# Kernel tuning notes

Hardware: AMD Instinct MI355X
Metric: run time of the kernel (lower is better)

## Reference

```python
import jax, jax.numpy as jnp
import numpy as np

LN_EPS = 1e-5


def setup_inputs() -> dict:
    key = jax.random.key(0)
    ks = jax.random.split(key, 4)
    B, N, E, H = 2, 512, 128, 256
    h = jax.random.normal(ks[0], (B, N, E), dtype=jnp.float32)
    gamma = jnp.ones((E,), dtype=jnp.float32)
    beta = jnp.zeros((E,), dtype=jnp.float32)
    # First Linear: in_dim = 2E, out_dim = H. Stored as [2E, H] (x @ W1 + b1).
    W1 = jax.random.normal(ks[1], (2 * E, H), dtype=jnp.float32) / np.sqrt(2 * E)
    b1 = jnp.zeros((H,), dtype=jnp.float32)
    # Second Linear: [H, 1] squeezed to [H], scalar bias.
    w2 = jax.random.normal(ks[2], (H,), dtype=jnp.float32) / np.sqrt(H)
    b2 = jnp.zeros((), dtype=jnp.float32)
    return {"h": h, "gamma": gamma, "beta": beta, "W1": W1, "b1": b1,
            "w2": w2, "b2": b2}


def reference(h, gamma, beta, W1, b1, w2, b2):
    # LayerNorm over E
    mu = jnp.mean(h, axis=-1, keepdims=True)
    var = jnp.mean(jnp.square(h - mu), axis=-1, keepdims=True)
    h_n = (h - mu) * jax.lax.rsqrt(var + LN_EPS) * gamma + beta  # [B,N,E]

    E = h_n.shape[-1]
    # Decompose Linear(concat(h_i, h_j)) = h_i @ Wa + h_j @ Wb + b1
    Wa, Wb = W1[:E], W1[E:]
    a = jnp.einsum('bne,eh->bnh', h_n, Wa)  # contribution of first slot
    b = jnp.einsum('bne,eh->bnh', h_n, Wb)  # contribution of second slot
    # Pairwise pre-activation for the (i,j) ordering: [B,N,N,H]
    z_ij = a[:, :, None, :] + b[:, None, :, :] + b1
    g = jax.nn.gelu(z_ij, approximate=False)  # torch GELU is exact (erf)
    l_ij = jnp.einsum('bijh,h->bij', g, w2) + b2  # [B,N,N]
    # l_ji[b,i,j] == l_ij[b,j,i], so reuse via transpose (same math as
    # running the MLP twice on swapped concat order).
    return 0.5 * (l_ij + jnp.swapaxes(l_ij, 1, 2))
```

## Files before the change

### kernel.cpp

```cpp
#include <hip/hip_runtime.h>
#include <math.h>

#define EDIM 128
#define HDIM 256
#define NDIM 512
#define BDIM 2
#define LN_EPS 1e-5f

typedef float v2f __attribute__((ext_vector_type(2)));

__global__ __launch_bounds__(256) void k_ln_proj(
    const float* __restrict__ hptr, const float* __restrict__ gamma,
    const float* __restrict__ beta, const float* __restrict__ W1,
    const float* __restrict__ b1, float* __restrict__ a_out,
    float* __restrict__ b_out)
{
    __shared__ float hn_s[4][EDIM];
    const int tid = threadIdx.x;
    const int r = tid >> 6;
    const int lane = tid & 63;
    const int row0 = blockIdx.x * 4;
    const float2 v = *(const float2*)(hptr + (row0 + r) * EDIM + lane * 2);
    float s  = v.x + v.y;
    float ss = v.x * v.x + v.y * v.y;
    #pragma unroll
    for (int k = 32; k >= 1; k >>= 1) {
        s  += __shfl_xor(s, k, 64);
        ss += __shfl_xor(ss, k, 64);
    }
    const float mu  = s * (1.0f / EDIM);
    const float var = ss * (1.0f / EDIM) - mu * mu;
    const float rs  = rsqrtf(var + LN_EPS);
    const float2 g2 = *(const float2*)(gamma + lane * 2);
    const float2 be = *(const float2*)(beta + lane * 2);
    hn_s[r][lane * 2]     = (v.x - mu) * rs * g2.x + be.x;
    hn_s[r][lane * 2 + 1] = (v.y - mu) * rs * g2.y + be.y;
    __syncthreads();
    float sa0 = 0.f, sa1 = 0.f, sa2 = 0.f, sa3 = 0.f;
    float sb0 = 0.f, sb1 = 0.f, sb2 = 0.f, sb3 = 0.f;
    #pragma unroll 4
    for (int e = 0; e < EDIM; ++e) {
        const float wa = W1[e * HDIM + tid];
        const float wb = W1[(EDIM + e) * HDIM + tid];
        const float h0 = hn_s[0][e], h1 = hn_s[1][e];
        const float h2 = hn_s[2][e], h3 = hn_s[3][e];
        sa0 = fmaf(h0, wa, sa0); sa1 = fmaf(h1, wa, sa1);
        sa2 = fmaf(h2, wa, sa2); sa3 = fmaf(h3, wa, sa3);
        sb0 = fmaf(h0, wb, sb0); sb1 = fmaf(h1, wb, sb1);
        sb2 = fmaf(h2, wb, sb2); sb3 = fmaf(h3, wb, sb3);
    }
    const float bb1 = b1[tid];
    a_out[(row0 + 0) * HDIM + tid] = sa0;
    a_out[(row0 + 1) * HDIM + tid] = sa1;
    a_out[(row0 + 2) * HDIM + tid] = sa2;
    a_out[(row0 + 3) * HDIM + tid] = sa3;
    b_out[(row0 + 0) * HDIM + tid] = sb0 + bb1;
    b_out[(row0 + 1) * HDIM + tid] = sb1 + bb1;
    b_out[(row0 + 2) * HDIM + tid] = sb2 + bb1;
    b_out[(row0 + 3) * HDIM + tid] = sb3 + bb1;
}

__device__ __forceinline__ v2f gelu2(v2f z) {
    const v2f c2 = {-0.10294826f, -0.10294826f};
    const v2f c1 = {-2.3022082f, -2.3022082f};
    const v2f z2 = z * z;
    const v2f q  = __builtin_elementwise_fma(c2, z2, c1);
    const v2f p  = z * q;
    v2f e;
    e.x = __builtin_amdgcn_exp2f(p.x);
    e.y = __builtin_amdgcn_exp2f(p.y);
    const v2f d = e + 1.0f;
    v2f r;
    r.x = __builtin_amdgcn_rcpf(d.x);
    r.y = __builtin_amdgcn_rcpf(d.y);
    return z * r;
}

#define HHALF 128
#define PAD 132

__global__ __launch_bounds__(256) void k_pair(
    const float* __restrict__ a, const float* __restrict__ bpb,
    const float* __restrict__ w2, const float* __restrict__ b2,
    float* __restrict__ out)
{
    __shared__ float a_s[32][PAD];
    __shared__ float b_s[16][PAD];
    __shared__ float w2_s[HDIM];
    const int blk = blockIdx.x;
    const int bb = blk >> 9;
    const int bi = (blk >> 5) & 15;
    const int bj = blk & 31;
    const int tid = threadIdx.x;

    const float* arow = a + (bb * NDIM + bi * 32) * HDIM;
    const float* brow = bpb + (bb * NDIM + bj * 16) * HDIM;

    if (tid < HDIM / 4) ((float4*)w2_s)[tid] = ((const float4*)w2)[tid];

    const int ti = tid >> 4, tj = tid & 15;
    const float* ap0 = a_s[ti];
    const float* ap1 = a_s[ti + 16];
    const float* bp  = b_s[tj];
    v2f acc0 = {0.f, 0.f}, acc1 = {0.f, 0.f};

    #pragma unroll
    for (int half = 0; half < 2; ++half) {
        if (half) __syncthreads();
        #pragma unroll
        for (int idx = tid; idx < 1536; idx += 256) {
            if (idx < 1024) {
                const int r = idx >> 5, c = idx & 31;
                *(float4*)&a_s[r][c * 4] =
                    *(const float4*)(arow + r * HDIM + half * HHALF + c * 4);
            } else {
                const int k = idx - 1024;
                const int r = k >> 5, c = k & 31;
                *(float4*)&b_s[r][c * 4] =
                    *(const float4*)(brow + r * HDIM + half * HHALF + c * 4);
            }
        }
        __syncthreads();
        const float* wp = w2_s + half * HHALF;
        #pragma unroll 4
        for (int hh = 0; hh < HHALF; hh += 4) {
            const float4 a0 = *(const float4*)(ap0 + hh);
            const float4 a1 = *(const float4*)(ap1 + hh);
            const float4 b0 = *(const float4*)(bp + hh);
            const float4 wv = *(const float4*)(wp + hh);
            const v2f alo0 = {a0.x, a0.y}, ahi0 = {a0.z, a0.w};
            const v2f alo1 = {a1.x, a1.y}, ahi1 = {a1.z, a1.w};
            const v2f blo  = {b0.x, b0.y}, bhi  = {b0.z, b0.w};
            const v2f wlo  = {wv.x, wv.y}, whi  = {wv.z, wv.w};
            acc0 = __builtin_elementwise_fma(wlo, gelu2(alo0 + blo), acc0);
            acc0 = __builtin_elementwise_fma(whi, gelu2(ahi0 + bhi), acc0);
            acc1 = __builtin_elementwise_fma(wlo, gelu2(alo1 + blo), acc1);
            acc1 = __builtin_elementwise_fma(whi, gelu2(ahi1 + bhi), acc1);
        }
    }
    const float bias = b2[0];
    const int i0 = bi * 32 + ti;
    const int j0 = bj * 16 + tj;
    float* ob = out + (bb * NDIM + i0) * NDIM + j0;
    ob[0]         = acc0.x + acc0.y + bias;
    ob[16 * NDIM] = acc1.x + acc1.y + bias;
}

__global__ __launch_bounds__(256) void k_sym(float* __restrict__ out) {
    __shared__ float Ta[32][33];
    __shared__ float Tb[32][33];
    const int blk = blockIdx.x;
    const int b  = blk >> 8;
    const int ti = (blk >> 4) & 15;
    const int tj = blk & 15;
    if (tj < ti) return;
    float* base = out + b * NDIM * NDIM;
    const int tx = threadIdx.x & 31;
    const int ty = threadIdx.x >> 5;
    #pragma unroll
    for (int r = ty; r < 32; r += 8) {
        Ta[r][tx] = base[(ti * 32 + r) * NDIM + tj * 32 + tx];
        Tb[r][tx] = base[(tj * 32 + r) * NDIM + ti * 32 + tx];
    }
    __syncthreads();
    #pragma unroll
    for (int r = ty; r < 32; r += 8) {
        base[(ti * 32 + r) * NDIM + tj * 32 + tx] = 0.5f * (Ta[r][tx] + Tb[tx][r]);
    }
    if (ti != tj) {
        #pragma unroll
        for (int r = ty; r < 32; r += 8) {
            base[(tj * 32 + r) * NDIM + ti * 32 + tx] = 0.5f * (Tb[r][tx] + Ta[tx][r]);
        }
    }
}

extern "C" void kernel_launch(void* const* d_in, const int* in_sizes, int n_in,
                              void* d_out, int out_size, void* d_ws, size_t ws_size,
                              hipStream_t stream) {
    const float* hptr  = (const float*)d_in[0];
    const float* gamma = (const float*)d_in[1];
    const float* beta  = (const float*)d_in[2];
    const float* W1    = (const float*)d_in[3];
    const float* b1    = (const float*)d_in[4];
    const float* w2    = (const float*)d_in[5];
    const float* b2    = (const float*)d_in[6];
    float* out = (float*)d_out;

    float* a_ws = (float*)d_ws;
    float* b_ws = a_ws + BDIM * NDIM * HDIM;

    k_ln_proj<<<(BDIM * NDIM) / 4, 256, 0, stream>>>(hptr, gamma, beta, W1, b1, a_ws, b_ws);
    k_pair<<<BDIM * 512, 256, 0, stream>>>(a_ws, b_ws, w2, b2, out);
    k_sym<<<BDIM * 256, 256, 0, stream>>>(out);
}
```

Before: 49.23 us.

## Split pair kernel over hidden halves with atomic accumulation into zeroed output

Each pair block now handles only one half of the hidden dimension, doubling the grid to 2048 blocks. Partial sums are combined with atomicAdd into an output that is zeroed by a memset first, and the scalar bias moves into the symmetrisation kernel. The aim is more parallelism and occupancy, with one smem load and no mid-loop barrier per block. The cost is an extra memset, atomic traffic, and floating-point summation order that is no longer deterministic.

```diff
diff --git a/kernel.cpp b/kernel.cpp
--- a/kernel.cpp
+++ b/kernel.cpp
@@ -79,24 +79,38 @@
 #define HHALF 128
 #define PAD 132
 
-__global__ __launch_bounds__(256) void k_pair(
+__global__ __launch_bounds__(256, 6) void k_pair(
     const float* __restrict__ a, const float* __restrict__ bpb,
-    const float* __restrict__ w2, const float* __restrict__ b2,
-    float* __restrict__ out)
+    const float* __restrict__ w2, float* __restrict__ out)
 {
     __shared__ float a_s[32][PAD];
     __shared__ float b_s[16][PAD];
-    __shared__ float w2_s[HDIM];
+    __shared__ float w2_s[HHALF];
     const int blk = blockIdx.x;
-    const int bb = blk >> 9;
-    const int bi = (blk >> 5) & 15;
-    const int bj = blk & 31;
+    const int hh = blk & 1;
+    const int bj = (blk >> 1) & 31;
+    const int bi = (blk >> 6) & 15;
+    const int bb = blk >> 10;
     const int tid = threadIdx.x;
+    const int hho = hh * HHALF;
 
-    const float* arow = a + (bb * NDIM + bi * 32) * HDIM;
-    const float* brow = bpb + (bb * NDIM + bj * 16) * HDIM;
+    const float* arow = a + (bb * NDIM + bi * 32) * HDIM + hho;
+    const float* brow = bpb + (bb * NDIM + bj * 16) * HDIM + hho;
 
-    if (tid < HDIM / 4) ((float4*)w2_s)[tid] = ((const float4*)w2)[tid];
+    if (tid < HHALF / 4) ((float4*)w2_s)[tid] = ((const float4*)(w2 + hho))[tid];
+
+    #pragma unroll
+    for (int idx = tid; idx < 1536; idx += 256) {
+        if (idx < 1024) {
+            const int r = idx >> 5, c = idx & 31;
+            *(float4*)&a_s[r][c * 4] = *(const float4*)(arow + r * HDIM + c * 4);
+        } else {
+            const int k = idx - 1024;
+            const int r = k >> 5, c = k & 31;
+            *(float4*)&b_s[r][c * 4] = *(const float4*)(brow + r * HDIM + c * 4);
+        }
+    }
+    __syncthreads();
 
     const int ti = tid >> 4, tj = tid & 15;
     const float* ap0 = a_s[ti];
@@ -104,49 +118,30 @@
     const float* bp  = b_s[tj];
     v2f acc0 = {0.f, 0.f}, acc1 = {0.f, 0.f};
 
-    #pragma unroll
-    for (int half = 0; half < 2; ++half) {
-        if (half) __syncthreads();
-        #pragma unroll
-        for (int idx = tid; idx < 1536; idx += 256) {
-            if (idx < 1024) {
-                const int r = idx >> 5, c = idx & 31;
-                *(float4*)&a_s[r][c * 4] =
-                    *(const float4*)(arow + r * HDIM + half * HHALF + c * 4);
-            } else {
-                const int k = idx - 1024;
-                const int r = k >> 5, c = k & 31;
-                *(float4*)&b_s[r][c * 4] =
-                    *(const float4*)(brow + r * HDIM + half * HHALF + c * 4);
-            }
-        }
-        __syncthreads();
-        const float* wp = w2_s + half * HHALF;
-        #pragma unroll 4
-        for (int hh = 0; hh < HHALF; hh += 4) {
-            const float4 a0 = *(const float4*)(ap0 + hh);
-            const float4 a1 = *(const float4*)(ap1 + hh);
-            const float4 b0 = *(const float4*)(bp + hh);
-            const float4 wv = *(const float4*)(wp + hh);
-            const v2f alo0 = {a0.x, a0.y}, ahi0 = {a0.z, a0.w};
-            const v2f alo1 = {a1.x, a1.y}, ahi1 = {a1.z, a1.w};
-            const v2f blo  = {b0.x, b0.y}, bhi  = {b0.z, b0.w};
-            const v2f wlo  = {wv.x, wv.y}, whi  = {wv.z, wv.w};
-            acc0 = __builtin_elementwise_fma(wlo, gelu2(alo0 + blo), acc0);
-            acc0 = __builtin_elementwise_fma(whi, gelu2(ahi0 + bhi), acc0);
-            acc1 = __builtin_elementwise_fma(wlo, gelu2(alo1 + blo), acc1);
-            acc1 = __builtin_elementwise_fma(whi, gelu2(ahi1 + bhi), acc1);
-        }
+    #pragma unroll 4
+    for (int h4 = 0; h4 < HHALF; h4 += 4) {
+        const float4 a0 = *(const float4*)(ap0 + h4);
+        const float4 a1 = *(const float4*)(ap1 + h4);
+        const float4 b0 = *(const float4*)(bp + h4);
+        const float4 wv = *(const float4*)(w2_s + h4);
+        const v2f alo0 = {a0.x, a0.y}, ahi0 = {a0.z, a0.w};
+        const v2f alo1 = {a1.x, a1.y}, ahi1 = {a1.z, a1.w};
+        const v2f blo  = {b0.x, b0.y}, bhi  = {b0.z, b0.w};
+        const v2f wlo  = {wv.x, wv.y}, whi  = {wv.z, wv.w};
+        acc0 = __builtin_elementwise_fma(wlo, gelu2(alo0 + blo), acc0);
+        acc0 = __builtin_elementwise_fma(whi, gelu2(ahi0 + bhi), acc0);
+        acc1 = __builtin_elementwise_fma(wlo, gelu2(alo1 + blo), acc1);
+        acc1 = __builtin_elementwise_fma(whi, gelu2(ahi1 + bhi), acc1);
     }
-    const float bias = b2[0];
     const int i0 = bi * 32 + ti;
     const int j0 = bj * 16 + tj;
     float* ob = out + (bb * NDIM + i0) * NDIM + j0;
-    ob[0]         = acc0.x + acc0.y + bias;
-    ob[16 * NDIM] = acc1.x + acc1.y + bias;
+    atomicAdd(ob,              acc0.x + acc0.y);
+    atomicAdd(ob + 16 * NDIM,  acc1.x + acc1.y);
 }
 
-__global__ __launch_bounds__(256) void k_sym(float* __restrict__ out) {
+__global__ __launch_bounds__(256) void k_sym(float* __restrict__ out,
+                                             const float* __restrict__ b2) {
     __shared__ float Ta[32][33];
     __shared__ float Tb[32][33];
     const int blk = blockIdx.x;
@@ -154,6 +149,7 @@
     const int ti = (blk >> 4) & 15;
     const int tj = blk & 15;
     if (tj < ti) return;
+    const float bias = b2[0];
     float* base = out + b * NDIM * NDIM;
     const int tx = threadIdx.x & 31;
     const int ty = threadIdx.x >> 5;
@@ -165,12 +161,12 @@
     __syncthreads();
     #pragma unroll
     for (int r = ty; r < 32; r += 8) {
-        base[(ti * 32 + r) * NDIM + tj * 32 + tx] = 0.5f * (Ta[r][tx] + Tb[tx][r]);
+        base[(ti * 32 + r) * NDIM + tj * 32 + tx] = 0.5f * (Ta[r][tx] + Tb[tx][r]) + bias;
     }
     if (ti != tj) {
         #pragma unroll
         for (int r = ty; r < 32; r += 8) {
-            base[(tj * 32 + r) * NDIM + ti * 32 + tx] = 0.5f * (Tb[r][tx] + Ta[tx][r]);
+            base[(tj * 32 + r) * NDIM + ti * 32 + tx] = 0.5f * (Tb[r][tx] + Ta[tx][r]) + bias;
         }
     }
 }
@@ -190,7 +186,9 @@
     float* a_ws = (float*)d_ws;
     float* b_ws = a_ws + BDIM * NDIM * HDIM;
 
+    hipMemsetAsync(d_out, 0, (size_t)out_size * sizeof(float), stream);
+
     k_ln_proj<<<(BDIM * NDIM) / 4, 256, 0, stream>>>(hptr, gamma, beta, W1, b1, a_ws, b_ws);
-    k_pair<<<BDIM * 512, 256, 0, stream>>>(a_ws, b_ws, w2, b2, out);
-    k_sym<<<BDIM * 256, 256, 0, stream>>>(out);
+    k_pair<<<BDIM * 16 * 32 * 2, 256, 0, stream>>>(a_ws, b_ws, w2, out);
+    k_sym<<<BDIM * 256, 256, 0, stream>>>(out, b2);
 }
```

After: 52.91 us. 1.07x slower.
